# Optimization experiments

Hardware: AMD Instinct MI355X
Metric: run time of the kernel (lower is better)

## Reference

```python
import jax, jax.numpy as jnp
import numpy as np

BOX_WARP = 1.2
BMIN, BMAX = -0.6, 0.6   # sampler bbox
EPS_FD = 0.01            # finite-difference eps for SDF normals
RADIUS = 0.5             # sphere sdf bias radius
INV_S = 80.0             # sdf -> density sharpness (softplus clamp mode)
S_PER_RAY = 96


def _grid_sample_one(feat, uv):
    # feat: [C,H,W]; uv: [M,2] in [-1,1]; bilinear, align_corners=False, zeros padding
    C, H, W = feat.shape
    x = ((uv[:, 0] + 1.0) * W - 1.0) * 0.5
    y = ((uv[:, 1] + 1.0) * H - 1.0) * 0.5
    x0 = jnp.floor(x).astype(jnp.int32)
    y0 = jnp.floor(y).astype(jnp.int32)
    wx = x - x0
    wy = y - y0

    def g(ix, iy):
        valid = ((ix >= 0) & (ix < W) & (iy >= 0) & (iy < H)).astype(feat.dtype)
        v = feat[:, jnp.clip(iy, 0, H - 1), jnp.clip(ix, 0, W - 1)]  # [C,M]
        return v * valid[None, :]

    out = (g(x0, y0) * (1 - wx) * (1 - wy) + g(x0 + 1, y0) * wx * (1 - wy)
           + g(x0, y0 + 1) * (1 - wx) * wy + g(x0 + 1, y0 + 1) * wx * wy)
    return out.T  # [M,C]


def sample_from_planes(planes, coords):
    # planes: [N,3,C,H,W]; coords: [N,M,3] -> [N,M,3*C]
    N, P, C, H, W = planes.shape
    M = coords.shape[1]
    nc = coords * (2.0 / BOX_WARP)
    proj = jnp.stack([nc[..., (0, 1)], nc[..., (0, 2)], nc[..., (1, 2)]], axis=1)  # [N,3,M,2]
    s = jax.vmap(_grid_sample_one)(planes.reshape(N * P, C, H, W), proj.reshape(N * P, M, 2))
    return s.reshape(N, P, M, C).transpose(0, 2, 1, 3).reshape(N, M, P * C)


def decode(planes, coords, W1, b1, W2, b2):
    x = sample_from_planes(planes, coords)
    return jax.nn.relu(x @ W1 + b1) @ W2 + b2  # [N,M,4]


def render(planes, ro, rd, W1, b1, W2, b2):
    N, R, _ = ro.shape
    S = S_PER_RAY
    safe_rd = jnp.where(jnp.abs(rd) < 1e-9, 1e-9, rd)
    t1 = (BMIN - ro) / safe_rd
    t2 = (BMAX - ro) / safe_rd
    tn = jnp.maximum(jnp.max(jnp.minimum(t1, t2), axis=-1), 0.0)   # [N,R] ray_start (auto box)
    tf = jnp.min(jnp.maximum(t1, t2), axis=-1)                      # [N,R] ray_end
    span = jnp.maximum(tf - tn, 0.0)
    frac = (jnp.arange(S, dtype=ro.dtype) + 0.5) / S
    depths = tn[..., None] + span[..., None] * frac                 # [N,R,S]
    pts = (ro[:, :, None, :] + depths[..., None] * rd[:, :, None, :]).reshape(N, R * S, 3)

    x = decode(planes, pts, W1, b1, W2, b2)
    sdf = x[..., 0:1]
    rgb = jax.nn.sigmoid(x[..., 1:]) * (1 + 2 * 0.001) - 0.001

    # finite-difference SDF gradient (3 extra decoder passes)
    eye = jnp.eye(3, dtype=pts.dtype) * EPS_FD
    sdf_off = jnp.stack(
        [decode(planes, jnp.clip(pts + eye[i], BMIN, BMAX), W1, b1, W2, b2)[..., 0] for i in range(3)],
        axis=-1)                                                    # [N,M,3]
    sdf_grad = (sdf_off - sdf) / EPS_FD
    normal = sdf_grad / (jnp.linalg.norm(sdf_grad, axis=-1, keepdims=True) + 1e-8)

    # sphere sdf bias, sdf -> density, alpha compositing
    shifted = sdf[..., 0] + (jnp.linalg.norm(pts, axis=-1) - RADIUS)
    sigma = jax.nn.softplus(-shifted * INV_S).reshape(N, R, S)
    delta = (span / S)[..., None]
    alpha = 1.0 - jnp.exp(-sigma * delta)
    T = jnp.cumprod(1.0 - alpha + 1e-10, axis=-1)
    T = jnp.concatenate([jnp.ones_like(T[..., :1]), T[..., :-1]], axis=-1)
    w = alpha * T                                                   # [N,R,S]

    rgb_s = (w[..., None] * rgb.reshape(N, R, S, 3)).sum(-2)
    wsum = w.sum(-1, keepdims=True)
    rgb_s = rgb_s + (1.0 - wsum)                                    # white background
    depth_s = (w * depths).sum(-1, keepdims=True)
    normal_s = (w[..., None] * normal.reshape(N, R, S, 3)).sum(-2)
    return rgb_s, depth_s, wsum, sdf_grad, normal_s


def reference(planes, ray_origins, ray_directions, W1, b1, W2, b2, render_size):
    N = planes.shape[0]
    rgb_s, depth_s, wsum, sdf_grad, normal_s = render(planes, ray_origins, ray_directions, W1, b1, W2, b2)
    n = normal_s / (jnp.linalg.norm(normal_s, axis=-1, keepdims=True) + 1e-8)
    n = (n + 1.0) * 0.5
    n = n * wsum  # lerp(0, n, opacity)
    H = W = render_size
    comp_rgb = rgb_s.transpose(0, 2, 1).reshape(N, 3, H, W)
    comp_depth = depth_s.transpose(0, 2, 1).reshape(N, 1, H, W)
    opacity = wsum.transpose(0, 2, 1).reshape(N, 1, H, W)
    comp_normal = n.transpose(0, 2, 1).reshape(N, 3, H, W)
    return (comp_rgb, comp_depth, opacity, comp_normal, sdf_grad)


def setup_inputs():
    key = jax.random.key(0)
    k0, k1, k2 = jax.random.split(key, 3)
    N, C, Hp, rs = 1, 80, 64, 64
    planes = jax.random.normal(k0, (N, 3, C, Hp, Hp), jnp.float32)
    u = jnp.linspace(-0.45, 0.45, rs)
    uu, vv = jnp.meshgrid(u, u, indexing='xy')
    d = jnp.stack([uu, vv, -jnp.ones_like(uu)], -1).reshape(-1, 3)
    d = d / jnp.linalg.norm(d, axis=-1, keepdims=True)
    ray_directions = jnp.broadcast_to(d, (N, rs * rs, 3)).astype(jnp.float32)
    ray_origins = jnp.broadcast_to(jnp.array([0.0, 0.0, 1.5], jnp.float32), (N, rs * rs, 3))
    W1 = jax.random.normal(k1, (3 * C, 64), jnp.float32) * 0.05
    b1 = jnp.zeros((64,), jnp.float32)
    W2 = jax.random.normal(k2, (64, 4), jnp.float32) * 0.05
    b2 = jnp.zeros((4,), jnp.float32)
    return {"planes": planes, "ray_origins": ray_origins, "ray_directions": ray_directions,
            "W1": W1, "b1": b1, "W2": W2, "b2": b2, "render_size": rs}
```

## Files before the change

kernel.cpp:

```cpp
#include <hip/hip_runtime.h>
#include <hip/hip_bf16.h>

#define NUM_RAYS 4096
#define S_PER 96
#define NPTS (NUM_RAYS * S_PER)
#define CCH 80
#define HID 64

#define WSB_W2     256
#define WSB_B1     1536
#define WSB_B2     1856
#define WSB_W1S    4096
#define WSB_PT     40960



typedef __attribute__((ext_vector_type(8))) short short8;
typedef __attribute__((ext_vector_type(4))) float f32x4;
typedef __attribute__((ext_vector_type(2))) float f32x2;

__device__ __forceinline__ float bf2f(__hip_bfloat16 v) { return __bfloat162float(v); }

__device__ __forceinline__ short f2bs(float f) {
  __hip_bfloat16 h = __float2bfloat16(f);
  short s; __builtin_memcpy(&s, &h, 2); return s;
}

template <bool BF16>
__device__ __forceinline__ float ldin(const void* p, size_t i) {
  if (BF16) return bf2f(((const __hip_bfloat16*)p)[i]);
  else      return ((const float*)p)[i];
}
template <bool BF16>
__device__ __forceinline__ void stout(void* p, size_t i, float v) {
  if (BF16) ((__hip_bfloat16*)p)[i] = __float2bfloat16(v);
  else      ((float*)p)[i] = v;
}

__device__ __forceinline__ f32x2 unpk2(unsigned u) {
  f32x2 r;
  r.x = __uint_as_float(u << 16);
  r.y = __uint_as_float(u);
  return r;
}

__device__ __forceinline__ unsigned pack_bf16(float lo, float hi) {
#if __has_builtin(__builtin_amdgcn_cvt_pk_bf16_f32)
  typedef __attribute__((ext_vector_type(2))) __bf16 b2t;
  b2t r = __builtin_amdgcn_cvt_pk_bf16_f32(lo, hi);
  unsigned u; __builtin_memcpy(&u, &r, 4); return u;
#else
  unsigned ul = __float_as_uint(lo) + 0x8000u;
  unsigned uh = __float_as_uint(hi) + 0x8000u;
  return __builtin_amdgcn_perm(uh, ul, 0x07060302);
#endif
}

__device__ __forceinline__ bool detect_bf16(const void* rdv) {
  int lane = threadIdx.x & 63;
  const __hip_bfloat16* p = (const __hip_bfloat16*)rdv;
  float x = bf2f(p[lane * 3 + 0]);
  float y = bf2f(p[lane * 3 + 1]);
  float z = bf2f(p[lane * 3 + 2]);
  float n2 = x * x + y * y + z * z;
  bool ok = (n2 > 0.95f) && (n2 < 1.05f);
  return __ballot(ok) == ~0ull;
}

template <bool BF16>
__device__ __forceinline__ void prep_body(const void* __restrict__ W1,
                                          const void* __restrict__ b1,
                                          const void* __restrict__ W2,
                                          const void* __restrict__ b2,
                                          float* __restrict__ ws) {
  int tid = blockIdx.x * blockDim.x + threadIdx.x;
  unsigned short* w1sw = (unsigned short*)((char*)ws + WSB_W1S);
  if (tid < 15360) {
    int p = tid / 5120;
    int r = tid - p * 5120;
    int ch, n;
    if (r < 4096) {
      int ccl  = r >> 11;
      int r2   = r & 2047;
      int j    = r2 & 7;
      int lane = (r2 >> 3) & 63;
      int nb   = r2 >> 9;
      ch = ccl * 32 + 8 * (lane >> 4) + j;
      n  = nb * 16 + (lane & 15);
    } else {
      int r2   = r - 4096;
      int j    = r2 & 7;
      int l31  = (r2 >> 3) & 31;
      int nb   = r2 >> 8;
      ch = 64 + 8 * (l31 >> 4) + j;
      n  = nb * 16 + (l31 & 15);
    }
    w1sw[tid] = (unsigned short)f2bs(ldin<BF16>(W1, (size_t)(p * 80 + ch) * 64 + n));
  }
  float* w2f = (float*)((char*)ws + WSB_W2);
  float* b1f = (float*)((char*)ws + WSB_B1);
  float* b2f = (float*)((char*)ws + WSB_B2);
  if (tid < 256) w2f[tid] = ldin<BF16>(W2, tid);
  if (tid < 64)  b1f[tid] = ldin<BF16>(b1, tid);
  if (tid < 4)   b2f[tid] = ldin<BF16>(b2, tid);
}

__global__ void prep_kernel(const void* __restrict__ W1,
                            const void* __restrict__ b1,
                            const void* __restrict__ W2,
                            const void* __restrict__ b2,
                            const void* __restrict__ rd,
                            float* __restrict__ ws) {
  if (detect_bf16(rd)) prep_body<true >(W1, b1, W2, b2, ws);
  else                 prep_body<false>(W1, b1, W2, b2, ws);
}

template <bool BF16>
__device__ __forceinline__ void transpose_body(const void* __restrict__ planes,
                                               float* __restrict__ ws) {
  int b  = blockIdx.x;
  int tt = b & 15;
  int ct = (b >> 4) % 5;
  int p  = b / 80;
  int tex = tt * 256 + threadIdx.x;
  unsigned u[8];
  #pragma unroll
  for (int i = 0; i < 8; i++) {
    int c0 = ct * 16 + 2 * i;
    float v0 = ldin<BF16>(planes, ((size_t)(p * 80 + c0) * 4096) + tex);
    float v1 = ldin<BF16>(planes, ((size_t)(p * 80 + c0 + 1) * 4096) + tex);
    unsigned s0 = (unsigned short)f2bs(v0);
    unsigned s1 = (unsigned short)f2bs(v1);
    u[i] = s0 | (s1 << 16);
  }
  unsigned short* ptb = (unsigned short*)((char*)ws + WSB_PT);
  uint4* dst = (uint4*)(ptb + ((size_t)(p * 4096 + tex) * 80 + ct * 16));
  dst[0] = make_uint4(u[0], u[1], u[2], u[3]);
  dst[1] = make_uint4(u[4], u[5], u[6], u[7]);
}

__global__ void transpose_kernel(const void* __restrict__ planes,
                                 const void* __restrict__ rd,
                                 float* __restrict__ ws) {
  if (detect_bf16(rd)) transpose_body<true >(planes, ws);
  else                 transpose_body<false>(planes, ws);
}

struct TapInfo {
  float w00, w10, w01, w11;
  int o00, o10, o01, o11;
};
__device__ __forceinline__ TapInfo tap_setup(float u, float v) {
  TapInfo t;
  float fx = u * 32.0f + 31.5f;
  float fy = v * 32.0f + 31.5f;
  float flx = floorf(fx), fly = floorf(fy);
  int x0 = (int)flx, y0 = (int)fly;
  float wx = fx - flx, wy = fy - fly;
  int x1 = x0 + 1, y1 = y0 + 1;
  bool vx0 = (x0 >= 0) && (x0 < 64);
  bool vx1 = (x1 >= 0) && (x1 < 64);
  bool vy0 = (y0 >= 0) && (y0 < 64);
  bool vy1 = (y1 >= 0) && (y1 < 64);
  int cx0 = min(max(x0, 0), 63), cx1 = min(max(x1, 0), 63);
  int cy0 = min(max(y0, 0), 63), cy1 = min(max(y1, 0), 63);
  t.w00 = (1.0f - wx) * (1.0f - wy) * ((vx0 && vy0) ? 1.0f : 0.0f);
  t.w10 = wx * (1.0f - wy)          * ((vx1 && vy0) ? 1.0f : 0.0f);
  t.w01 = (1.0f - wx) * wy          * ((vx0 && vy1) ? 1.0f : 0.0f);
  t.w11 = wx * wy                   * ((vx1 && vy1) ? 1.0f : 0.0f);
  t.o00 = cy0 * 64 + cx0; t.o10 = cy0 * 64 + cx1;
  t.o01 = cy1 * 64 + cx0; t.o11 = cy1 * 64 + cx1;
  return t;
}

template <bool BF16>
__device__ __forceinline__ void fused_body(const void* __restrict__ ro,
                                           const void* __restrict__ rd,
                                           const float* __restrict__ ws,
                                           void* __restrict__ out,
                                           unsigned short* __restrict__ w1s,
                                           float (*__restrict__ rec)[7],
                                           float* __restrict__ w2s,
                                           float* __restrict__ xfer,
                                           float (*__restrict__ red)[8]) {
  const unsigned short* ptb = (const unsigned short*)((const char*)ws + WSB_PT);
  const float* w2f = (const float*)((const char*)ws + WSB_W2);
  const float* b1f = (const float*)((const char*)ws + WSB_B1);
  const float* b2f = (const float*)((const char*)ws + WSB_B2);

  int tid = threadIdx.x;
  int wave = tid >> 6;
  int lane = tid & 63;
  int lane15 = lane & 15;
  int quad = lane >> 4;
  int ray = blockIdx.x;

  {
    const uint4* src = (const uint4*)((const char*)ws + WSB_W1S);
    uint4* dst = (uint4*)w1s;
    #pragma unroll
    for (int t = 0; t < 8; t++) {
      int idx = tid + 256 * t;
      if (idx < 1920) dst[idx] = src[idx];
    }
  }
  if (tid < 256) w2s[tid] = w2f[tid];

  float ox = ldin<BF16>(ro, (size_t)ray*3+0), oy = ldin<BF16>(ro, (size_t)ray*3+1), oz = ldin<BF16>(ro, (size_t)ray*3+2);
  float dx = ldin<BF16>(rd, (size_t)ray*3+0), dy = ldin<BF16>(rd, (size_t)ray*3+1), dz = ldin<BF16>(rd, (size_t)ray*3+2);
  float o3[3] = {ox, oy, oz}, d3[3] = {dx, dy, dz};
  float tmin = -1e30f, tmax = 1e30f;
  #pragma unroll
  for (int k = 0; k < 3; k++) {
    float sd = (fabsf(d3[k]) < 1e-9f) ? 1e-9f : d3[k];
    float ta = (-0.6f - o3[k]) / sd;
    float tb = ( 0.6f - o3[k]) / sd;
    tmin = fmaxf(tmin, fminf(ta, tb));
    tmax = fminf(tmax, fmaxf(ta, tb));
  }
  float tn = fmaxf(tmin, 0.0f);
  float span = fmaxf(tmax - tn, 0.0f);
  float delta = span * (1.0f / (float)S_PER);
  float b1x[4];
  #pragma unroll
  for (int nb = 0; nb < 4; nb++) b1x[nb] = b1f[nb * 16 + lane15];

  __syncthreads();

  #pragma unroll 1
  for (int it = 0; it < 6; it++) {
    int sbase = it * 16 + wave * 4;

    int sF = sbase + (lane15 >> 2);
    int d  = lane15 & 3;
    float depF = tn + span * (((float)sF + 0.5f) * (1.0f / (float)S_PER));
    float px = ox + depF * dx, py = oy + depF * dy, pz = oz + depF * dz;
    if (d == 1) px += 0.01f;
    if (d == 2) py += 0.01f;
    if (d == 3) pz += 0.01f;
    if (d > 0) {
      px = fminf(fmaxf(px, -0.6f), 0.6f);
      py = fminf(fmaxf(py, -0.6f), 0.6f);
      pz = fminf(fmaxf(pz, -0.6f), 0.6f);
    }
    const float inv = 1.0f / 0.6f;
    float ux = px * inv, uy = py * inv, uz = pz * inv;

    f32x4 acc[4];
    #pragma unroll
    for (int nb = 0; nb < 4; nb++) acc[nb] = (f32x4){0.f, 0.f, 0.f, 0.f};

    #pragma unroll 1
    for (int p = 0; p < 3; p++) {
      float u = (p == 2) ? uy : ux;
      float v = (p == 0) ? uy : uz;
      TapInfo t = tap_setup(u, v);
      const unsigned short* c00p = ptb + (size_t)p * 327680 + t.o00 * 80 + 8 * quad;
      const unsigned short* c10p = ptb + (size_t)p * 327680 + t.o10 * 80 + 8 * quad;
      const unsigned short* c01p = ptb + (size_t)p * 327680 + t.o01 * 80 + 8 * quad;
      const unsigned short* c11p = ptb + (size_t)p * 327680 + t.o11 * 80 + 8 * quad;
      f32x2 wv00 = {t.w00, t.w00}, wv10 = {t.w10, t.w10};
      f32x2 wv01 = {t.w01, t.w01}, wv11 = {t.w11, t.w11};
      const unsigned short* w1p = w1s + p * 5120;
      #pragma unroll
      for (int ccl = 0; ccl < 3; ccl++) {
        int4 afi = {0, 0, 0, 0};
        if (ccl < 2 || quad < 2) {
          uint4 q00 = *(const uint4*)(c00p + 32 * ccl);
          uint4 q10 = *(const uint4*)(c10p + 32 * ccl);
          uint4 q01 = *(const uint4*)(c01p + 32 * ccl);
          uint4 q11 = *(const uint4*)(c11p + 32 * ccl);
          unsigned u00[4] = {q00.x, q00.y, q00.z, q00.w};
          unsigned u10[4] = {q10.x, q10.y, q10.z, q10.w};
          unsigned u01[4] = {q01.x, q01.y, q01.z, q01.w};
          unsigned u11[4] = {q11.x, q11.y, q11.z, q11.w};
          int ae[4];
          #pragma unroll
          for (int q = 0; q < 4; q++) {
            f32x2 f = unpk2(u00[q]) * wv00;
            f = __builtin_elementwise_fma(unpk2(u10[q]), wv10, f);
            f = __builtin_elementwise_fma(unpk2(u01[q]), wv01, f);
            f = __builtin_elementwise_fma(unpk2(u11[q]), wv11, f);
            ae[q] = (int)pack_bf16(f.x, f.y);
          }
          afi.x = ae[0]; afi.y = ae[1]; afi.z = ae[2]; afi.w = ae[3];
        }
        short8 afr;
        __builtin_memcpy(&afr, &afi, 16);
        #pragma unroll
        for (int nb = 0; nb < 4; nb++) {
          int boff = (ccl < 2) ? (ccl * 2048 + (nb * 64 + lane) * 8)
                               : (4096 + (nb * 32 + (lane & 31)) * 8);
          short8 bfr = *(const short8*)(w1p + boff);
          acc[nb] = __builtin_amdgcn_mfma_f32_16x16x32_bf16(afr, bfr, acc[nb], 0, 0, 0);
        }
      }
    }

    float vals[7];
    #pragma unroll
    for (int k = 0; k < 7; k++) vals[k] = 0.0f;
    #pragma unroll
    for (int nb = 0; nb < 4; nb++) {
      float4 w2r = *(const float4*)(w2s + (nb * 16 + lane15) * 4);
      float hr0 = fmaxf(acc[nb][0] + b1x[nb], 0.0f);
      vals[0] = fmaf(hr0, w2r.x, vals[0]);
      vals[4] = fmaf(hr0, w2r.y, vals[4]);
      vals[5] = fmaf(hr0, w2r.z, vals[5]);
      vals[6] = fmaf(hr0, w2r.w, vals[6]);
      float hr1 = fmaxf(acc[nb][1] + b1x[nb], 0.0f);
      float hr2 = fmaxf(acc[nb][2] + b1x[nb], 0.0f);
      float hr3 = fmaxf(acc[nb][3] + b1x[nb], 0.0f);
      vals[1] = fmaf(hr1, w2r.x, vals[1]);
      vals[2] = fmaf(hr2, w2r.x, vals[2]);
      vals[3] = fmaf(hr3, w2r.x, vals[3]);
    }
    #pragma unroll
    for (int mask = 1; mask < 16; mask <<= 1) {
      #pragma unroll
      for (int k = 0; k < 7; k++) vals[k] += __shfl_xor(vals[k], mask, 64);
    }

    if (lane15 == 0) {
      int sE = sbase + quad;
      #pragma unroll
      for (int k = 0; k < 7; k++) rec[sE][k] = vals[k];
    }
  }

  __syncthreads();

  float b2_0 = b2f[0], b2_1 = b2f[1], b2_2 = b2f[2], b2_3 = b2f[3];
  float a = 0.f, l = 0.f, pcr = 0.f, pcg = 0.f, pcb = 0.f, pnx = 0.f, pny = 0.f, pnz = 0.f, pdt = 0.f;
  if (tid < S_PER) {
    float v0 = rec[tid][0], v1 = rec[tid][1], v2 = rec[tid][2], v3 = rec[tid][3];
    float v4 = rec[tid][4], v5 = rec[tid][5], v6 = rec[tid][6];
    float sdf0 = v0 + b2_0;
    float g0 = (v1 - v0) * 100.0f;
    float g1 = (v2 - v0) * 100.0f;
    float g2 = (v3 - v0) * 100.0f;
    size_t gid = (size_t)ray * S_PER + tid;
    stout<BF16>(out, (size_t)32768 + gid * 3 + 0, g0);
    stout<BF16>(out, (size_t)32768 + gid * 3 + 1, g1);
    stout<BF16>(out, (size_t)32768 + gid * 3 + 2, g2);
    pcr = 1.0f / (1.0f + expf(-(v4 + b2_1))) * 1.002f - 0.001f;
    pcg = 1.0f / (1.0f + expf(-(v5 + b2_2))) * 1.002f - 0.001f;
    pcb = 1.0f / (1.0f + expf(-(v6 + b2_3))) * 1.002f - 0.001f;
    pdt = tn + span * (((float)tid + 0.5f) * (1.0f / (float)S_PER));
    float ex = ox + pdt * dx, ey = oy + pdt * dy, ez = oz + pdt * dz;
    float pn = sqrtf(ex * ex + ey * ey + ez * ez);
    float shifted = sdf0 + pn - 0.5f;
    float xarg = -shifted * 80.0f;
    float sigma = (xarg > 20.0f) ? xarg : log1pf(expf(xarg));
    a = 1.0f - expf(-sigma * delta);
    float gl = sqrtf(g0 * g0 + g1 * g1 + g2 * g2) + 1e-8f;
    float igl = 1.0f / gl;
    pnx = g0 * igl; pny = g1 * igl; pnz = g2 * igl;
    l = logf(1.0f - a + 1e-10f);
  }

  float lv = l;
  #pragma unroll
  for (int off = 1; off < 64; off <<= 1) {
    float up = __shfl_up(lv, off, 64);
    if (lane >= off) lv += up;
  }
  if (tid == 63) xfer[0] = lv;
  __syncthreads();
  if (tid >= 64 && tid < S_PER) lv += xfer[0];

  float T = expf(lv - l);
  float w = (tid < S_PER) ? a * T : 0.0f;
  float q[8];
  q[0] = w;
  q[1] = w * pcr; q[2] = w * pcg; q[3] = w * pcb;
  q[4] = w * pnx; q[5] = w * pny; q[6] = w * pnz;
  q[7] = w * pdt;
  #pragma unroll
  for (int off = 1; off < 64; off <<= 1) {
    #pragma unroll
    for (int k = 0; k < 8; k++) q[k] += __shfl_xor(q[k], off, 64);
  }
  if (lane == 0) {
    #pragma unroll
    for (int k = 0; k < 8; k++) red[wave][k] = q[k];
  }
  __syncthreads();
  if (tid == 0) {
    float R[8];
    #pragma unroll
    for (int k = 0; k < 8; k++) R[k] = red[0][k] + red[1][k] + red[2][k] + red[3][k];
    float wsum = R[0];
    float nl = sqrtf(R[4] * R[4] + R[5] * R[5] + R[6] * R[6]) + 1e-8f;
    float inl = 1.0f / nl;
    float nrm3[3] = {R[4], R[5], R[6]};
    float rgb3[3] = {R[1], R[2], R[3]};
    #pragma unroll
    for (int c = 0; c < 3; c++) {
      float n = (nrm3[c] * inl + 1.0f) * 0.5f * wsum;
      stout<BF16>(out, (size_t)(c * 4096 + ray), rgb3[c] + 1.0f - wsum);
      stout<BF16>(out, (size_t)(20480 + c * 4096 + ray), n);
    }
    stout<BF16>(out, (size_t)(12288 + ray), R[7]);
    stout<BF16>(out, (size_t)(16384 + ray), wsum);
  }
}

__global__ __launch_bounds__(256) void fused_kernel(
    const void* __restrict__ ro,
    const void* __restrict__ rd,
    const float* __restrict__ ws,
    void* __restrict__ out) {
  __shared__ __align__(16) unsigned short w1s[15360];
  __shared__ float rec[S_PER][7];
  __shared__ float w2s[256];
  __shared__ float xfer[1];
  __shared__ float red[4][8];

  if (detect_bf16(rd)) fused_body<true >(ro, rd, ws, out, w1s, rec, w2s, xfer, red);
  else                 fused_body<false>(ro, rd, ws, out, w1s, rec, w2s, xfer, red);
}

extern "C" void kernel_launch(void* const* d_in, const int* in_sizes, int n_in,
                              void* d_out, int out_size, void* d_ws, size_t ws_size,
                              hipStream_t stream) {
  const void* planes = d_in[0];
  const void* ro     = d_in[1];
  const void* rd     = d_in[2];
  const void* W1     = d_in[3];
  const void* b1     = d_in[4];
  const void* W2     = d_in[5];
  const void* b2     = d_in[6];
  float* ws = (float*)d_ws;

  prep_kernel<<<64, 256, 0, stream>>>(W1, b1, W2, b2, rd, ws);
  transpose_kernel<<<240, 256, 0, stream>>>(planes, rd, ws);
  fused_kernel<<<NUM_RAYS, 256, 0, stream>>>(ro, rd, ws, d_out);
}
```

Before: 270.5 us.

## Process two rays per block and merge setup kernels into one launch

The fused kernel now runs 512 threads per block, handling two rays per block, so the 30KB W1 copy into shared memory is amortized over two rays. The prep and transpose kernels are merged into a single setup launch to remove one launch and its gap. Per-ray shared buffers are duplicated and indexed by half. Larger blocks and more threads sharing the same barriers may reduce scheduling flexibility and occupancy granularity.

```diff
diff --git a/kernel.cpp b/kernel.cpp
--- a/kernel.cpp
+++ b/kernel.cpp
@@ -72,8 +72,7 @@
                                           const void* __restrict__ b1,
                                           const void* __restrict__ W2,
                                           const void* __restrict__ b2,
-                                          float* __restrict__ ws) {
-  int tid = blockIdx.x * blockDim.x + threadIdx.x;
+                                          float* __restrict__ ws, int tid) {
   unsigned short* w1sw = (unsigned short*)((char*)ws + WSB_W1S);
   if (tid < 15360) {
     int p = tid / 5120;
@@ -105,16 +104,6 @@
   if (tid < 4)   b2f[tid] = ldin<BF16>(b2, tid);
 }
 
-__global__ void prep_kernel(const void* __restrict__ W1,
-                            const void* __restrict__ b1,
-                            const void* __restrict__ W2,
-                            const void* __restrict__ b2,
-                            const void* __restrict__ rd,
-                            float* __restrict__ ws) {
-  if (detect_bf16(rd)) prep_body<true >(W1, b1, W2, b2, ws);
-  else                 prep_body<false>(W1, b1, W2, b2, ws);
-}
-
 template <bool BF16>
 __device__ __forceinline__ void transpose_body(const void* __restrict__ planes,
                                                float* __restrict__ ws) {
@@ -139,11 +128,22 @@
   dst[1] = make_uint4(u[4], u[5], u[6], u[7]);
 }
 
-__global__ void transpose_kernel(const void* __restrict__ planes,
-                                 const void* __restrict__ rd,
-                                 float* __restrict__ ws) {
-  if (detect_bf16(rd)) transpose_body<true >(planes, ws);
-  else                 transpose_body<false>(planes, ws);
+__global__ void setup_kernel(const void* __restrict__ planes,
+                             const void* __restrict__ W1,
+                             const void* __restrict__ b1,
+                             const void* __restrict__ W2,
+                             const void* __restrict__ b2,
+                             const void* __restrict__ rd,
+                             float* __restrict__ ws) {
+  bool bf = detect_bf16(rd);
+  if (blockIdx.x < 240) {
+    if (bf) transpose_body<true >(planes, ws);
+    else    transpose_body<false>(planes, ws);
+  } else {
+    int tid = (blockIdx.x - 240) * 256 + threadIdx.x;
+    if (bf) prep_body<true >(W1, b1, W2, b2, ws, tid);
+    else    prep_body<false>(W1, b1, W2, b2, ws, tid);
+  }
 }
 
 struct TapInfo {
@@ -179,28 +179,30 @@
                                            const float* __restrict__ ws,
                                            void* __restrict__ out,
                                            unsigned short* __restrict__ w1s,
-                                           float (*__restrict__ rec)[7],
+                                           float (*__restrict__ rec)[S_PER][7],
                                            float* __restrict__ w2s,
                                            float* __restrict__ xfer,
-                                           float (*__restrict__ red)[8]) {
+                                           float (*__restrict__ red)[4][8]) {
   const unsigned short* ptb = (const unsigned short*)((const char*)ws + WSB_PT);
   const float* w2f = (const float*)((const char*)ws + WSB_W2);
   const float* b1f = (const float*)((const char*)ws + WSB_B1);
   const float* b2f = (const float*)((const char*)ws + WSB_B2);
 
   int tid = threadIdx.x;
-  int wave = tid >> 6;
+  int half = tid >> 8;
+  int t   = tid & 255;
+  int wave = t >> 6;
   int lane = tid & 63;
   int lane15 = lane & 15;
   int quad = lane >> 4;
-  int ray = blockIdx.x;
+  int ray = blockIdx.x * 2 + half;
 
   {
     const uint4* src = (const uint4*)((const char*)ws + WSB_W1S);
     uint4* dst = (uint4*)w1s;
     #pragma unroll
-    for (int t = 0; t < 8; t++) {
-      int idx = tid + 256 * t;
+    for (int it = 0; it < 4; it++) {
+      int idx = tid + 512 * it;
       if (idx < 1920) dst[idx] = src[idx];
     }
   }
@@ -254,13 +256,13 @@
     for (int p = 0; p < 3; p++) {
       float u = (p == 2) ? uy : ux;
       float v = (p == 0) ? uy : uz;
-      TapInfo t = tap_setup(u, v);
-      const unsigned short* c00p = ptb + (size_t)p * 327680 + t.o00 * 80 + 8 * quad;
-      const unsigned short* c10p = ptb + (size_t)p * 327680 + t.o10 * 80 + 8 * quad;
-      const unsigned short* c01p = ptb + (size_t)p * 327680 + t.o01 * 80 + 8 * quad;
-      const unsigned short* c11p = ptb + (size_t)p * 327680 + t.o11 * 80 + 8 * quad;
-      f32x2 wv00 = {t.w00, t.w00}, wv10 = {t.w10, t.w10};
-      f32x2 wv01 = {t.w01, t.w01}, wv11 = {t.w11, t.w11};
+      TapInfo tp = tap_setup(u, v);
+      const unsigned short* c00p = ptb + (size_t)p * 327680 + tp.o00 * 80 + 8 * quad;
+      const unsigned short* c10p = ptb + (size_t)p * 327680 + tp.o10 * 80 + 8 * quad;
+      const unsigned short* c01p = ptb + (size_t)p * 327680 + tp.o01 * 80 + 8 * quad;
+      const unsigned short* c11p = ptb + (size_t)p * 327680 + tp.o11 * 80 + 8 * quad;
+      f32x2 wv00 = {tp.w00, tp.w00}, wv10 = {tp.w10, tp.w10};
+      f32x2 wv01 = {tp.w01, tp.w01}, wv11 = {tp.w11, tp.w11};
       const unsigned short* w1p = w1s + p * 5120;
       #pragma unroll
       for (int ccl = 0; ccl < 3; ccl++) {
@@ -324,7 +326,7 @@
     if (lane15 == 0) {
       int sE = sbase + quad;
       #pragma unroll
-      for (int k = 0; k < 7; k++) rec[sE][k] = vals[k];
+      for (int k = 0; k < 7; k++) rec[half][sE][k] = vals[k];
     }
   }
 
@@ -332,21 +334,21 @@
 
   float b2_0 = b2f[0], b2_1 = b2f[1], b2_2 = b2f[2], b2_3 = b2f[3];
   float a = 0.f, l = 0.f, pcr = 0.f, pcg = 0.f, pcb = 0.f, pnx = 0.f, pny = 0.f, pnz = 0.f, pdt = 0.f;
-  if (tid < S_PER) {
-    float v0 = rec[tid][0], v1 = rec[tid][1], v2 = rec[tid][2], v3 = rec[tid][3];
-    float v4 = rec[tid][4], v5 = rec[tid][5], v6 = rec[tid][6];
+  if (t < S_PER) {
+    float v0 = rec[half][t][0], v1 = rec[half][t][1], v2 = rec[half][t][2], v3 = rec[half][t][3];
+    float v4 = rec[half][t][4], v5 = rec[half][t][5], v6 = rec[half][t][6];
     float sdf0 = v0 + b2_0;
     float g0 = (v1 - v0) * 100.0f;
     float g1 = (v2 - v0) * 100.0f;
     float g2 = (v3 - v0) * 100.0f;
-    size_t gid = (size_t)ray * S_PER + tid;
+    size_t gid = (size_t)ray * S_PER + t;
     stout<BF16>(out, (size_t)32768 + gid * 3 + 0, g0);
     stout<BF16>(out, (size_t)32768 + gid * 3 + 1, g1);
     stout<BF16>(out, (size_t)32768 + gid * 3 + 2, g2);
     pcr = 1.0f / (1.0f + expf(-(v4 + b2_1))) * 1.002f - 0.001f;
     pcg = 1.0f / (1.0f + expf(-(v5 + b2_2))) * 1.002f - 0.001f;
     pcb = 1.0f / (1.0f + expf(-(v6 + b2_3))) * 1.002f - 0.001f;
-    pdt = tn + span * (((float)tid + 0.5f) * (1.0f / (float)S_PER));
+    pdt = tn + span * (((float)t + 0.5f) * (1.0f / (float)S_PER));
     float ex = ox + pdt * dx, ey = oy + pdt * dy, ez = oz + pdt * dz;
     float pn = sqrtf(ex * ex + ey * ey + ez * ez);
     float shifted = sdf0 + pn - 0.5f;
@@ -365,12 +367,12 @@
     float up = __shfl_up(lv, off, 64);
     if (lane >= off) lv += up;
   }
-  if (tid == 63) xfer[0] = lv;
+  if (t == 63) xfer[half] = lv;
   __syncthreads();
-  if (tid >= 64 && tid < S_PER) lv += xfer[0];
+  if (t >= 64 && t < S_PER) lv += xfer[half];
 
   float T = expf(lv - l);
-  float w = (tid < S_PER) ? a * T : 0.0f;
+  float w = (t < S_PER) ? a * T : 0.0f;
   float q[8];
   q[0] = w;
   q[1] = w * pcr; q[2] = w * pcg; q[3] = w * pcb;
@@ -383,13 +385,14 @@
   }
   if (lane == 0) {
     #pragma unroll
-    for (int k = 0; k < 8; k++) red[wave][k] = q[k];
+    for (int k = 0; k < 8; k++) red[half][wave][k] = q[k];
   }
   __syncthreads();
-  if (tid == 0) {
+  if (t == 0) {
     float R[8];
     #pragma unroll
-    for (int k = 0; k < 8; k++) R[k] = red[0][k] + red[1][k] + red[2][k] + red[3][k];
+    for (int k = 0; k < 8; k++)
+      R[k] = red[half][0][k] + red[half][1][k] + red[half][2][k] + red[half][3][k];
     float wsum = R[0];
     float nl = sqrtf(R[4] * R[4] + R[5] * R[5] + R[6] * R[6]) + 1e-8f;
     float inl = 1.0f / nl;
@@ -406,16 +409,16 @@
   }
 }
 
-__global__ __launch_bounds__(256) void fused_kernel(
+__global__ __launch_bounds__(512) void fused_kernel(
     const void* __restrict__ ro,
     const void* __restrict__ rd,
     const float* __restrict__ ws,
     void* __restrict__ out) {
   __shared__ __align__(16) unsigned short w1s[15360];
-  __shared__ float rec[S_PER][7];
+  __shared__ float rec[2][S_PER][7];
   __shared__ float w2s[256];
-  __shared__ float xfer[1];
-  __shared__ float red[4][8];
+  __shared__ float xfer[2];
+  __shared__ float red[2][4][8];
 
   if (detect_bf16(rd)) fused_body<true >(ro, rd, ws, out, w1s, rec, w2s, xfer, red);
   else                 fused_body<false>(ro, rd, ws, out, w1s, rec, w2s, xfer, red);
@@ -433,7 +436,6 @@
   const void* b2     = d_in[6];
   float* ws = (float*)d_ws;
 
-  prep_kernel<<<64, 256, 0, stream>>>(W1, b1, W2, b2, rd, ws);
-  transpose_kernel<<<240, 256, 0, stream>>>(planes, rd, ws);
-  fused_kernel<<<NUM_RAYS, 256, 0, stream>>>(ro, rd, ws, d_out);
-}
+  setup_kernel<<<304, 256, 0, stream>>>(planes, W1, b1, W2, b2, rd, ws);
+  fused_kernel<<<NUM_RAYS / 2, 512, 0, stream>>>(ro, rd, ws, d_out);
+}
```

New measurement: 324.6 us. 1.2x slower.

## Run MFMA per bilinear tap and blend outputs; merge setup kernels

Applied to the files above, without the earlier changes.

Bilinear interpolation is no longer done in VALU before the MFMA. The four raw bf16 tap vectors are now fed to four separate MFMA accumulator sets, and the tap weights are applied to the outputs via shuffled weights, relying on linearity of the first layer. This removes the unpack/fma/pack VALU work but quadruples MFMA count and accumulator registers, which may reduce occupancy. The prep and transpose kernels are also merged into one launch.

```diff
diff --git a/kernel.cpp b/kernel.cpp
--- a/kernel.cpp
+++ b/kernel.cpp
@@ -17,7 +17,6 @@
 
 typedef __attribute__((ext_vector_type(8))) short short8;
 typedef __attribute__((ext_vector_type(4))) float f32x4;
-typedef __attribute__((ext_vector_type(2))) float f32x2;
 
 __device__ __forceinline__ float bf2f(__hip_bfloat16 v) { return __bfloat162float(v); }
 
@@ -35,25 +34,6 @@
 __device__ __forceinline__ void stout(void* p, size_t i, float v) {
   if (BF16) ((__hip_bfloat16*)p)[i] = __float2bfloat16(v);
   else      ((float*)p)[i] = v;
-}
-
-__device__ __forceinline__ f32x2 unpk2(unsigned u) {
-  f32x2 r;
-  r.x = __uint_as_float(u << 16);
-  r.y = __uint_as_float(u);
-  return r;
-}
-
-__device__ __forceinline__ unsigned pack_bf16(float lo, float hi) {
-#if __has_builtin(__builtin_amdgcn_cvt_pk_bf16_f32)
-  typedef __attribute__((ext_vector_type(2))) __bf16 b2t;
-  b2t r = __builtin_amdgcn_cvt_pk_bf16_f32(lo, hi);
-  unsigned u; __builtin_memcpy(&u, &r, 4); return u;
-#else
-  unsigned ul = __float_as_uint(lo) + 0x8000u;
-  unsigned uh = __float_as_uint(hi) + 0x8000u;
-  return __builtin_amdgcn_perm(uh, ul, 0x07060302);
-#endif
 }
 
 __device__ __forceinline__ bool detect_bf16(const void* rdv) {
@@ -72,8 +52,7 @@
                                           const void* __restrict__ b1,
                                           const void* __restrict__ W2,
                                           const void* __restrict__ b2,
-                                          float* __restrict__ ws) {
-  int tid = blockIdx.x * blockDim.x + threadIdx.x;
+                                          float* __restrict__ ws, int tid) {
   unsigned short* w1sw = (unsigned short*)((char*)ws + WSB_W1S);
   if (tid < 15360) {
     int p = tid / 5120;
@@ -105,16 +84,6 @@
   if (tid < 4)   b2f[tid] = ldin<BF16>(b2, tid);
 }
 
-__global__ void prep_kernel(const void* __restrict__ W1,
-                            const void* __restrict__ b1,
-                            const void* __restrict__ W2,
-                            const void* __restrict__ b2,
-                            const void* __restrict__ rd,
-                            float* __restrict__ ws) {
-  if (detect_bf16(rd)) prep_body<true >(W1, b1, W2, b2, ws);
-  else                 prep_body<false>(W1, b1, W2, b2, ws);
-}
-
 template <bool BF16>
 __device__ __forceinline__ void transpose_body(const void* __restrict__ planes,
                                                float* __restrict__ ws) {
@@ -139,11 +108,22 @@
   dst[1] = make_uint4(u[4], u[5], u[6], u[7]);
 }
 
-__global__ void transpose_kernel(const void* __restrict__ planes,
-                                 const void* __restrict__ rd,
-                                 float* __restrict__ ws) {
-  if (detect_bf16(rd)) transpose_body<true >(planes, ws);
-  else                 transpose_body<false>(planes, ws);
+__global__ void setup_kernel(const void* __restrict__ planes,
+                             const void* __restrict__ W1,
+                             const void* __restrict__ b1,
+                             const void* __restrict__ W2,
+                             const void* __restrict__ b2,
+                             const void* __restrict__ rd,
+                             float* __restrict__ ws) {
+  bool bf = detect_bf16(rd);
+  if (blockIdx.x < 240) {
+    if (bf) transpose_body<true >(planes, ws);
+    else    transpose_body<false>(planes, ws);
+  } else {
+    int tid = (blockIdx.x - 240) * 256 + threadIdx.x;
+    if (bf) prep_body<true >(W1, b1, W2, b2, ws, tid);
+    else    prep_body<false>(W1, b1, W2, b2, ws, tid);
+  }
 }
 
 struct TapInfo {
@@ -246,55 +226,74 @@
     const float inv = 1.0f / 0.6f;
     float ux = px * inv, uy = py * inv, uz = pz * inv;
 
-    f32x4 acc[4];
-    #pragma unroll
-    for (int nb = 0; nb < 4; nb++) acc[nb] = (f32x4){0.f, 0.f, 0.f, 0.f};
+    f32x4 tot[4];
+    #pragma unroll
+    for (int nb = 0; nb < 4; nb++) tot[nb] = (f32x4){0.f, 0.f, 0.f, 0.f};
 
     #pragma unroll 1
     for (int p = 0; p < 3; p++) {
       float u = (p == 2) ? uy : ux;
       float v = (p == 0) ? uy : uz;
-      TapInfo t = tap_setup(u, v);
-      const unsigned short* c00p = ptb + (size_t)p * 327680 + t.o00 * 80 + 8 * quad;
-      const unsigned short* c10p = ptb + (size_t)p * 327680 + t.o10 * 80 + 8 * quad;
-      const unsigned short* c01p = ptb + (size_t)p * 327680 + t.o01 * 80 + 8 * quad;
-      const unsigned short* c11p = ptb + (size_t)p * 327680 + t.o11 * 80 + 8 * quad;
-      f32x2 wv00 = {t.w00, t.w00}, wv10 = {t.w10, t.w10};
-      f32x2 wv01 = {t.w01, t.w01}, wv11 = {t.w11, t.w11};
+      TapInfo tp = tap_setup(u, v);
+      const unsigned short* c00p = ptb + (size_t)p * 327680 + tp.o00 * 80 + 8 * quad;
+      const unsigned short* c10p = ptb + (size_t)p * 327680 + tp.o10 * 80 + 8 * quad;
+      const unsigned short* c01p = ptb + (size_t)p * 327680 + tp.o01 * 80 + 8 * quad;
+      const unsigned short* c11p = ptb + (size_t)p * 327680 + tp.o11 * 80 + 8 * quad;
       const unsigned short* w1p = w1s + p * 5120;
+
+      f32x4 a0[4], a1[4], a2[4], a3[4];
+      #pragma unroll
+      for (int nb = 0; nb < 4; nb++) {
+        a0[nb] = (f32x4){0.f, 0.f, 0.f, 0.f};
+        a1[nb] = (f32x4){0.f, 0.f, 0.f, 0.f};
+        a2[nb] = (f32x4){0.f, 0.f, 0.f, 0.f};
+        a3[nb] = (f32x4){0.f, 0.f, 0.f, 0.f};
+      }
+
       #pragma unroll
       for (int ccl = 0; ccl < 3; ccl++) {
-        int4 afi = {0, 0, 0, 0};
+        uint4 q00 = {0, 0, 0, 0}, q10 = {0, 0, 0, 0}, q01 = {0, 0, 0, 0}, q11 = {0, 0, 0, 0};
         if (ccl < 2 || quad < 2) {
-          uint4 q00 = *(const uint4*)(c00p + 32 * ccl);
-          uint4 q10 = *(const uint4*)(c10p + 32 * ccl);
-          uint4 q01 = *(const uint4*)(c01p + 32 * ccl);
-          uint4 q11 = *(const uint4*)(c11p + 32 * ccl);
-          unsigned u00[4] = {q00.x, q00.y, q00.z, q00.w};
-          unsigned u10[4] = {q10.x, q10.y, q10.z, q10.w};
-          unsigned u01[4] = {q01.x, q01.y, q01.z, q01.w};
-          unsigned u11[4] = {q11.x, q11.y, q11.z, q11.w};
-          int ae[4];
-          #pragma unroll
-          for (int q = 0; q < 4; q++) {
-            f32x2 f = unpk2(u00[q]) * wv00;
-            f = __builtin_elementwise_fma(unpk2(u10[q]), wv10, f);
-            f = __builtin_elementwise_fma(unpk2(u01[q]), wv01, f);
-            f = __builtin_elementwise_fma(unpk2(u11[q]), wv11, f);
-            ae[q] = (int)pack_bf16(f.x, f.y);
-          }
-          afi.x = ae[0]; afi.y = ae[1]; afi.z = ae[2]; afi.w = ae[3];
+          q00 = *(const uint4*)(c00p + 32 * ccl);
+          q10 = *(const uint4*)(c10p + 32 * ccl);
+          q01 = *(const uint4*)(c01p + 32 * ccl);
+          q11 = *(const uint4*)(c11p + 32 * ccl);
         }
-        short8 afr;
-        __builtin_memcpy(&afr, &afi, 16);
+        short8 f00, f10, f01, f11;
+        __builtin_memcpy(&f00, &q00, 16);
+        __builtin_memcpy(&f10, &q10, 16);
+        __builtin_memcpy(&f01, &q01, 16);
+        __builtin_memcpy(&f11, &q11, 16);
         #pragma unroll
         for (int nb = 0; nb < 4; nb++) {
           int boff = (ccl < 2) ? (ccl * 2048 + (nb * 64 + lane) * 8)
                                : (4096 + (nb * 32 + (lane & 31)) * 8);
           short8 bfr = *(const short8*)(w1p + boff);
-          acc[nb] = __builtin_amdgcn_mfma_f32_16x16x32_bf16(afr, bfr, acc[nb], 0, 0, 0);
+          a0[nb] = __builtin_amdgcn_mfma_f32_16x16x32_bf16(f00, bfr, a0[nb], 0, 0, 0);
+          a1[nb] = __builtin_amdgcn_mfma_f32_16x16x32_bf16(f10, bfr, a1[nb], 0, 0, 0);
+          a2[nb] = __builtin_amdgcn_mfma_f32_16x16x32_bf16(f01, bfr, a2[nb], 0, 0, 0);
+          a3[nb] = __builtin_amdgcn_mfma_f32_16x16x32_bf16(f11, bfr, a3[nb], 0, 0, 0);
         }
       }
+
+      f32x4 wv00, wv10, wv01, wv11;
+      #pragma unroll
+      for (int reg = 0; reg < 4; reg++) {
+        int src = (lane & 48) + 4 * quad + reg;
+        wv00[reg] = __shfl(tp.w00, src, 64);
+        wv10[reg] = __shfl(tp.w10, src, 64);
+        wv01[reg] = __shfl(tp.w01, src, 64);
+        wv11[reg] = __shfl(tp.w11, src, 64);
+      }
+      #pragma unroll
+      for (int nb = 0; nb < 4; nb++) {
+        f32x4 s = tot[nb];
+        s = __builtin_elementwise_fma(a0[nb], wv00, s);
+        s = __builtin_elementwise_fma(a1[nb], wv10, s);
+        s = __builtin_elementwise_fma(a2[nb], wv01, s);
+        s = __builtin_elementwise_fma(a3[nb], wv11, s);
+        tot[nb] = s;
+      }
     }
 
     float vals[7];
@@ -303,14 +302,14 @@
     #pragma unroll
     for (int nb = 0; nb < 4; nb++) {
       float4 w2r = *(const float4*)(w2s + (nb * 16 + lane15) * 4);
-      float hr0 = fmaxf(acc[nb][0] + b1x[nb], 0.0f);
+      float hr0 = fmaxf(tot[nb][0] + b1x[nb], 0.0f);
       vals[0] = fmaf(hr0, w2r.x, vals[0]);
       vals[4] = fmaf(hr0, w2r.y, vals[4]);
       vals[5] = fmaf(hr0, w2r.z, vals[5]);
       vals[6] = fmaf(hr0, w2r.w, vals[6]);
-      float hr1 = fmaxf(acc[nb][1] + b1x[nb], 0.0f);
-      float hr2 = fmaxf(acc[nb][2] + b1x[nb], 0.0f);
-      float hr3 = fmaxf(acc[nb][3] + b1x[nb], 0.0f);
+      float hr1 = fmaxf(tot[nb][1] + b1x[nb], 0.0f);
+      float hr2 = fmaxf(tot[nb][2] + b1x[nb], 0.0f);
+      float hr3 = fmaxf(tot[nb][3] + b1x[nb], 0.0f);
       vals[1] = fmaf(hr1, w2r.x, vals[1]);
       vals[2] = fmaf(hr2, w2r.x, vals[2]);
       vals[3] = fmaf(hr3, w2r.x, vals[3]);
@@ -433,7 +432,6 @@
   const void* b2     = d_in[6];
   float* ws = (float*)d_ws;
 
-  prep_kernel<<<64, 256, 0, stream>>>(W1, b1, W2, b2, rd, ws);
-  transpose_kernel<<<240, 256, 0, stream>>>(planes, rd, ws);
+  setup_kernel<<<304, 256, 0, stream>>>(planes, W1, b1, W2, b2, rd, ws);
   fused_kernel<<<NUM_RAYS, 256, 0, stream>>>(ro, rd, ws, d_out);
 }
```

After: 349.0 us. 29.0% more time.
